# Kernel optimization log

Hardware: AMD Instinct MI355X
Metric: run time of the kernel (lower is better)

Reference implementation:

```python
import jax, jax.numpy as jnp
import numpy as np


def _edt(mask):
    """Exact Euclidean distance transform of a binary [H,W] mask.

    Matches scipy.ndimage.distance_transform_edt: for nonzero pixels,
    distance to the nearest zero pixel (0 at zero pixels).
    Two-pass exact algorithm: 1D distance along rows (axis 0) per column,
    then D[i,j] = min_k d1[i,k]^2 + (j-k)^2 (Felzenszwalb-Huttenlocher identity).
    """
    H, W = mask.shape
    BIG = jnp.float32(H + W)  # larger than any real pixel distance
    zero = mask == 0
    idx = jnp.arange(H, dtype=jnp.float32)[:, None]  # [H,1]
    # nearest zero above (inclusive)
    up = jax.lax.cummax(jnp.where(zero, idx, -BIG), axis=0)
    d_up = idx - up
    # nearest zero below (inclusive): cummin from the bottom
    dn = -jnp.flip(jax.lax.cummax(jnp.flip(jnp.where(zero, -idx, -2 * BIG), axis=0), axis=0), axis=0)
    d_dn = dn - idx
    d1 = jnp.minimum(jnp.minimum(d_up, d_dn), BIG)  # [H,W] 1D column distance
    d1sq = d1 * d1
    j = jnp.arange(W, dtype=jnp.float32)
    off = (j[:, None] - j[None, :]) ** 2  # [W,W], off[j,k]
    # D[i,j] = min_k d1sq[i,k] + (j-k)^2
    Dsq = jnp.min(d1sq[:, None, :] + off[None, :, :], axis=-1)  # [H,W]
    return jnp.sqrt(Dsq)


def _phi_level_set(mask):
    """Normalized signed distance map for one [H,W] binary mask."""
    dist_inside = _edt(mask)
    dist_outside = _edt(1.0 - mask)
    phi = dist_outside - dist_inside
    denom = jnp.max(jnp.abs(phi)) + 1e-8
    return jnp.where(jnp.any(mask > 0), phi / denom, jnp.zeros_like(phi))


def _combined_loss(predictions, targets):
    probs = jax.nn.sigmoid(predictions)
    # Dice
    p = probs.reshape(-1)
    t = targets.reshape(-1)
    smooth = 1e-6
    inter = jnp.sum(p * t)
    dice = 1.0 - (2.0 * inter + smooth) / (jnp.sum(p) + jnp.sum(t) + smooth)
    # Boundary: phi is computed from detached targets (constant)
    masks = jax.lax.stop_gradient(targets)[:, 0]  # [B,H,W]
    phi = jax.vmap(_phi_level_set)(masks)[:, None]  # [B,1,H,W]
    boundary = jnp.mean(phi * probs)
    # BCE with logits (numerically stable)
    x = predictions
    bce = jnp.mean(jnp.clip(x, 0.0, None) - x * targets + jnp.log1p(jnp.exp(-jnp.abs(x))))
    # rebalance schedule at epoch 0: alpha = initial_alpha = 0.005
    alpha = 0.005
    beta = max(0.0, 0.6 - alpha)
    return (1.0 - beta) * dice + beta * boundary + 0.4 * bce


def setup_inputs() -> dict:
    key = jax.random.key(0)
    k1, k2 = jax.random.split(key)
    B, C, H, W = 16, 1, 256, 256
    predictions = jax.random.normal(k1, (B, C, H, W), dtype=jnp.float32)
    targets = (jax.random.uniform(k2, (B, C, H, W)) < 0.3).astype(jnp.float32)
    return {"predictions": predictions, "targets": targets}


def reference(predictions, targets):
    return _combined_loss(predictions, targets)
```

## Files before the change

kernel.cpp:

```cpp
#include <hip/hip_runtime.h>
#include <math.h>

#define BB 16
#define HH 256
#define WW 256
#define NPIX (BB*HH*WW)
#define CH 16
#define RPC 16
#define ROWS 8
#define NRB (BB*HH/ROWS)
#define PADW 4
#define GSTRIDE (WW + 2*PADW)


__global__ __launch_bounds__(256) void fused_kernel(const float* __restrict__ pred,
                                                    const float4* __restrict__ targ4,
                                                    float* __restrict__ partials,
                                                    unsigned* __restrict__ flag,
                                                    float* __restrict__ out) {
    int g = blockIdx.x;
    int b = g >> 5;
    int r0 = (g & 31) << 3;
    int C = r0 >> 4;
    int rb0 = r0 & 15;
    int j = threadIdx.x;

    __shared__ unsigned short zbS[CH][WW];
    __shared__ float gg[ROWS][2][GSTRIDE];
    __shared__ float red[4][8];
    __shared__ float arrF[256][3];
    __shared__ float bnd[BB];
    __shared__ float wred[4][4];
    __shared__ unsigned lastBlk;

    const float4* img = targ4 + (size_t)b * HH * (WW / 4);
    #pragma unroll
    for (int k = 0; k < 4; ++k) {
        int T = (k << 8) + j;
        int c = T >> 6, q = T & 63;
        const float4* m = img + (c * RPC) * (WW / 4) + q;
        unsigned z0 = 0, z1 = 0, z2 = 0, z3 = 0;
        #pragma unroll
        for (int r = 0; r < RPC; ++r) {
            float4 v = m[r * (WW / 4)];
            if (v.x == 0.0f) z0 |= 1u << r;
            if (v.y == 0.0f) z1 |= 1u << r;
            if (v.z == 0.0f) z2 |= 1u << r;
            if (v.w == 0.0f) z3 |= 1u << r;
        }
        ushort4 o;
        o.x = (unsigned short)z0; o.y = (unsigned short)z1;
        o.z = (unsigned short)z2; o.w = (unsigned short)z3;
        *reinterpret_cast<ushort4*>(&zbS[c][q << 2]) = o;
    }
    if (j < 2 * ROWS * 2 * PADW) {
        int r = j >> 4, f = (j >> 3) & 1, p = j & 7;
        gg[r][f][(p < PADW) ? p : (WW + p)] = 1e30f;
    }
    __syncthreads();

    int la0 = -1, la1 = -1;
    int fb0 = 100000, fb1 = 100000;
    unsigned zoc = 0;
    #pragma unroll
    for (int c = 0; c < CH; ++c) {
        unsigned z = (unsigned)zbS[c][j];
        unsigned zi = (~z) & 0xFFFFu;
        if (c < C) {
            if (z)  la0 = (c << 4) + (31 - __clz(z));
            if (zi) la1 = (c << 4) + (31 - __clz(zi));
        } else if (c > C) {
            if (z  && fb0 == 100000) fb0 = (c << 4) + (__ffs(z) - 1);
            if (zi && fb1 == 100000) fb1 = (c << 4) + (__ffs(zi) - 1);
        } else {
            zoc = z;
        }
    }
    unsigned zoc1 = (~zoc) & 0xFFFFu;

    float x[ROWS];
    #pragma unroll
    for (int r = 0; r < ROWS; ++r)
        x[r] = pred[(((b << 8) + (r0 + r)) << 8) + j];

    #pragma unroll
    for (int r = 0; r < ROWS; ++r) {
        int rb = rb0 + r;
        int i = r0 + r;
        unsigned below = zoc & ((2u << rb) - 1u);
        int lz = below ? ((C << 4) + (31 - __clz(below))) : la0;
        unsigned above = zoc & (0xFFFFu & ~((1u << rb) - 1u));
        int fz = above ? ((C << 4) + (__ffs(above) - 1)) : fb0;
        int da = (lz < 0) ? 100000 : (i - lz);
        int d0 = min(min(da, fz - i), 512);
        float f0 = (float)d0;
        gg[r][0][PADW + j] = f0 * f0;
        unsigned below1 = zoc1 & ((2u << rb) - 1u);
        int lz1 = below1 ? ((C << 4) + (31 - __clz(below1))) : la1;
        unsigned above1 = zoc1 & (0xFFFFu & ~((1u << rb) - 1u));
        int fz1 = above1 ? ((C << 4) + (__ffs(above1) - 1)) : fb1;
        int da1 = (lz1 < 0) ? 100000 : (i - lz1);
        int d1v = min(min(da1, fz1 - i), 512);
        float f1 = (float)d1v;
        gg[r][1][PADW + j] = f1 * f1;
    }
    __syncthreads();

    float sp = 0.f, st = 0.f, spt = 0.f, sbce = 0.f, sphip = 0.f, amax = 0.f;
    #pragma unroll
    for (int r = 0; r < ROWS; ++r) {
        int rb = rb0 + r;
        bool msk = (((zoc >> rb) & 1u) == 0u);
        const float* bsel = &gg[r][msk ? 0 : 1][0];
        float best = 1e30f;
        #pragma unroll
        for (int c = 0; c <= 2 * PADW; ++c) {
            float Cc = (float)((PADW - c) * (PADW - c));
            best = fminf(best, bsel[j + c] + Cc);
        }
        if (__any(best > 25.0f)) {
            const float* bs = bsel + PADW;
            for (int k = 0; k < WW; ++k) {
                float df = (float)(j - k);
                best = fminf(best, bs[k] + df * df);
            }
        }
        float dd = sqrtf(best);
        float phi = msk ? -dd : dd;
        float xr = x[r];
        float ax = fabsf(xr);
        float q = __expf(-ax);
        float pa = 1.0f / (1.0f + q);
        float p = (xr >= 0.0f) ? pa : q * pa;
        sp += p;
        st += msk ? 1.0f : 0.0f;
        spt += msk ? p : 0.0f;
        sbce += fmaxf(xr, 0.0f) - (msk ? xr : 0.0f) - __logf(pa);
        sphip += phi * p;
        amax = fmaxf(amax, fabsf(phi));
    }

    #pragma unroll
    for (int off = 32; off > 0; off >>= 1) {
        sp    += __shfl_down(sp,    off, 64);
        st    += __shfl_down(st,    off, 64);
        spt   += __shfl_down(spt,   off, 64);
        sbce  += __shfl_down(sbce,  off, 64);
        sphip += __shfl_down(sphip, off, 64);
        amax   = fmaxf(amax,  __shfl_down(amax,  off, 64));
    }
    int lane = j & 63, wv = j >> 6;
    if (lane == 0) {
        red[wv][0] = sp; red[wv][1] = st; red[wv][2] = spt; red[wv][3] = sbce;
        red[wv][4] = sphip; red[wv][5] = amax;
    }
    __syncthreads();

    if (j == 0) {
        float* o = partials + (g << 3);
        #pragma unroll
        for (int q2 = 0; q2 < 5; ++q2)
            o[q2] = red[0][q2] + red[1][q2] + red[2][q2] + red[3][q2];
        o[5] = fmaxf(fmaxf(red[0][5], red[1][5]), fmaxf(red[2][5], red[3][5]));
        __builtin_amdgcn_fence(__ATOMIC_RELEASE, "agent");
        unsigned prev = atomicAdd(flag, 1u);
        lastBlk = (prev == (unsigned)(NRB - 1)) ? 1u : 0u;
    }
    __syncthreads();
    if (lastBlk) {
        __builtin_amdgcn_fence(__ATOMIC_ACQUIRE, "agent");
        int t = j;
        float s0 = 0.f, s1 = 0.f, s2 = 0.f, s3 = 0.f, s4 = 0.f, m5 = 0.f;
        #pragma unroll
        for (int e = 0; e < 2; ++e) {
            const float* rec = partials + (((t << 1) + e) << 3);
            s0 += rec[0]; s1 += rec[1]; s2 += rec[2]; s3 += rec[3];
            s4 += rec[4];
            m5 = fmaxf(m5, rec[5]);
        }
        arrF[t][0] = s4; arrF[t][1] = m5; arrF[t][2] = s1;
        __syncthreads();
        if (t < 16) {
            float Sb = 0.f, Mb = 0.f, STb = 0.f;
            for (int e = 0; e < 16; ++e) {
                Sb += arrF[t * 16 + e][0];
                Mb = fmaxf(Mb, arrF[t * 16 + e][1]);
                STb += arrF[t * 16 + e][2];
            }
            bnd[t] = (STb > 0.0f) ? (Sb / (Mb + 1e-8f)) : 0.0f;
        }
        #pragma unroll
        for (int off = 32; off > 0; off >>= 1) {
            s0 += __shfl_down(s0, off, 64);
            s1 += __shfl_down(s1, off, 64);
            s2 += __shfl_down(s2, off, 64);
            s3 += __shfl_down(s3, off, 64);
        }
        int lane2 = t & 63, wv2 = t >> 6;
        if (lane2 == 0) { wred[wv2][0] = s0; wred[wv2][1] = s1; wred[wv2][2] = s2; wred[wv2][3] = s3; }
        __syncthreads();
        if (t == 0) {
            float sp2   = wred[0][0] + wred[1][0] + wred[2][0] + wred[3][0];
            float st2   = wred[0][1] + wred[1][1] + wred[2][1] + wred[3][1];
            float spt2  = wred[0][2] + wred[1][2] + wred[2][2] + wred[3][2];
            float sbce2 = wred[0][3] + wred[1][3] + wred[2][3] + wred[3][3];
            float sbnd = 0.f;
            #pragma unroll
            for (int bb2 = 0; bb2 < BB; ++bb2) sbnd += bnd[bb2];
            float dice = 1.0f - (2.0f * spt2 + 1e-6f) / (sp2 + st2 + 1e-6f);
            float invN = 1.0f / (float)NPIX;
            float boundary = sbnd * invN;
            float bce = sbce2 * invN;
            float alpha = 0.005f;
            float beta = 0.6f - alpha;
            out[0] = (1.0f - beta) * dice + beta * boundary + 0.4f * bce;
        }
    }
}

extern "C" void kernel_launch(void* const* d_in, const int* in_sizes, int n_in,
                              void* d_out, int out_size, void* d_ws, size_t ws_size,
                              hipStream_t stream) {
    (void)in_sizes; (void)n_in; (void)out_size; (void)ws_size;
    const float* pred = (const float*)d_in[0];
    const float* targ = (const float*)d_in[1];
    float* partials = (float*)d_ws;
    unsigned* flag = (unsigned*)((char*)d_ws + NRB * 8 * sizeof(float));

    hipMemsetAsync(flag, 0, sizeof(unsigned), stream);
    fused_kernel<<<NRB, 256, 0, stream>>>(pred, (const float4*)targ, partials, flag, (float*)d_out);
}
```

Measured before the change: 79.16 us.

## Precompute column zero bitmasks in a separate kernel instead of per-block rebuild

Splits the fused kernel into a small kernel that packs the target mask into 16-row zero bitmasks once per image, and a main kernel that reads these bitmasks from global memory. This removes the 32x redundant reading of each full target image by every row block. The bitmask kernel also resets the completion flag, replacing the separate memset. It adds a second kernel launch and a global round trip for the bitmask.

```diff
diff --git a/kernel.cpp b/kernel.cpp
--- a/kernel.cpp
+++ b/kernel.cpp
@@ -13,11 +13,33 @@
 #define GSTRIDE (WW + 2*PADW)
 
 
-__global__ __launch_bounds__(256) void fused_kernel(const float* __restrict__ pred,
-                                                    const float4* __restrict__ targ4,
-                                                    float* __restrict__ partials,
-                                                    unsigned* __restrict__ flag,
-                                                    float* __restrict__ out) {
+__global__ __launch_bounds__(64) void zbuild_kernel(const float4* __restrict__ targ4,
+                                                    ushort4* __restrict__ zb4,
+                                                    unsigned* __restrict__ flag) {
+    int blk = blockIdx.x;
+    int t = threadIdx.x;
+    if (blk == 0 && t == 0) *flag = 0u;
+    const float4* m = targ4 + (size_t)blk * RPC * (WW / 4) + t;
+    unsigned z0 = 0, z1 = 0, z2 = 0, z3 = 0;
+    #pragma unroll
+    for (int r = 0; r < RPC; ++r) {
+        float4 v = m[r * (WW / 4)];
+        if (v.x == 0.0f) z0 |= 1u << r;
+        if (v.y == 0.0f) z1 |= 1u << r;
+        if (v.z == 0.0f) z2 |= 1u << r;
+        if (v.w == 0.0f) z3 |= 1u << r;
+    }
+    ushort4 o;
+    o.x = (unsigned short)z0; o.y = (unsigned short)z1;
+    o.z = (unsigned short)z2; o.w = (unsigned short)z3;
+    zb4[blk * (WW / 4) + t] = o;
+}
+
+__global__ __launch_bounds__(256) void rowmin_fused_kernel(const unsigned short* __restrict__ zb,
+                                                           const float* __restrict__ pred,
+                                                           float* __restrict__ partials,
+                                                           unsigned* __restrict__ flag,
+                                                           float* __restrict__ out) {
     int g = blockIdx.x;
     int b = g >> 5;
     int r0 = (g & 31) << 3;
@@ -25,46 +47,12 @@
     int rb0 = r0 & 15;
     int j = threadIdx.x;
 
-    __shared__ unsigned short zbS[CH][WW];
-    __shared__ float gg[ROWS][2][GSTRIDE];
-    __shared__ float red[4][8];
-    __shared__ float arrF[256][3];
-    __shared__ float bnd[BB];
-    __shared__ float wred[4][4];
-    __shared__ unsigned lastBlk;
-
-    const float4* img = targ4 + (size_t)b * HH * (WW / 4);
-    #pragma unroll
-    for (int k = 0; k < 4; ++k) {
-        int T = (k << 8) + j;
-        int c = T >> 6, q = T & 63;
-        const float4* m = img + (c * RPC) * (WW / 4) + q;
-        unsigned z0 = 0, z1 = 0, z2 = 0, z3 = 0;
-        #pragma unroll
-        for (int r = 0; r < RPC; ++r) {
-            float4 v = m[r * (WW / 4)];
-            if (v.x == 0.0f) z0 |= 1u << r;
-            if (v.y == 0.0f) z1 |= 1u << r;
-            if (v.z == 0.0f) z2 |= 1u << r;
-            if (v.w == 0.0f) z3 |= 1u << r;
-        }
-        ushort4 o;
-        o.x = (unsigned short)z0; o.y = (unsigned short)z1;
-        o.z = (unsigned short)z2; o.w = (unsigned short)z3;
-        *reinterpret_cast<ushort4*>(&zbS[c][q << 2]) = o;
-    }
-    if (j < 2 * ROWS * 2 * PADW) {
-        int r = j >> 4, f = (j >> 3) & 1, p = j & 7;
-        gg[r][f][(p < PADW) ? p : (WW + p)] = 1e30f;
-    }
-    __syncthreads();
-
     int la0 = -1, la1 = -1;
     int fb0 = 100000, fb1 = 100000;
     unsigned zoc = 0;
     #pragma unroll
     for (int c = 0; c < CH; ++c) {
-        unsigned z = (unsigned)zbS[c][j];
+        unsigned z = (unsigned)zb[((b * CH + c) << 8) + j];
         unsigned zi = (~z) & 0xFFFFu;
         if (c < C) {
             if (z)  la0 = (c << 4) + (31 - __clz(z));
@@ -82,6 +70,17 @@
     #pragma unroll
     for (int r = 0; r < ROWS; ++r)
         x[r] = pred[(((b << 8) + (r0 + r)) << 8) + j];
+
+    __shared__ float gg[ROWS][2][GSTRIDE];
+    __shared__ float red[4][8];
+    __shared__ float arrF[256][3];
+    __shared__ float bnd[BB];
+    __shared__ float wred[4][4];
+    __shared__ unsigned lastBlk;
+    if (j < 2 * ROWS * 2 * PADW) {
+        int r = j >> 4, f = (j >> 3) & 1, p = j & 7;
+        gg[r][f][(p < PADW) ? p : (WW + p)] = 1e30f;
+    }
 
     #pragma unroll
     for (int r = 0; r < ROWS; ++r) {
@@ -224,9 +223,10 @@
     (void)in_sizes; (void)n_in; (void)out_size; (void)ws_size;
     const float* pred = (const float*)d_in[0];
     const float* targ = (const float*)d_in[1];
-    float* partials = (float*)d_ws;
-    unsigned* flag = (unsigned*)((char*)d_ws + NRB * 8 * sizeof(float));
-
-    hipMemsetAsync(flag, 0, sizeof(unsigned), stream);
-    fused_kernel<<<NRB, 256, 0, stream>>>(pred, (const float4*)targ, partials, flag, (float*)d_out);
+    unsigned short* zb = (unsigned short*)d_ws;
+    float* partials = (float*)((char*)d_ws + BB * CH * WW * sizeof(unsigned short));
+    unsigned* flag = (unsigned*)((char*)partials + NRB * 8 * sizeof(float));
+
+    zbuild_kernel<<<BB * CH, 64, 0, stream>>>((const float4*)targ, (ushort4*)zb, flag);
+    rowmin_fused_kernel<<<NRB, 256, 0, stream>>>(zb, pred, partials, flag, (float*)d_out);
 }
```

New measurement: 75.44 us. 1.05x faster.
